# Performance work log

Hardware: AMD Instinct MI355X
Metric: run time of the kernel (lower is better)

Reference implementation:

```python
import jax, jax.numpy as jnp
import numpy as np

N, C, V, T = 256, 256, 25, 20
K = 3            # kernel_size
PAD = 1          # padding
O = 256          # out_channels
C4 = C // 4
EPS = 1e-5


def _bn(x, p, axes_shape):
    # p: (4, dim) = gamma, beta, running_mean, running_var (eval-mode BN)
    g, b, m, v = (p[i].reshape(axes_shape) for i in range(4))
    return (x - m) * (g / jnp.sqrt(v + EPS)) + b


def setup_inputs() -> dict:
    key = jax.random.key(0)
    ks = jax.random.split(key, 12)
    rn = lambda k, s, sc=0.05: jax.random.normal(k, s, jnp.float32) * sc
    bn = lambda k, d: jnp.stack([
        1.0 + 0.1 * jax.random.normal(jax.random.fold_in(k, 0), (d,), jnp.float32),  # gamma
        0.1 * jax.random.normal(jax.random.fold_in(k, 1), (d,), jnp.float32),        # beta
        0.1 * jax.random.normal(jax.random.fold_in(k, 2), (d,), jnp.float32),        # mean
        0.5 + jax.random.uniform(jax.random.fold_in(k, 3), (d,), jnp.float32),       # var
    ])
    return {
        "x": jax.random.normal(ks[0], (N, C, V, T), jnp.float32),
        "Wg1": rn(ks[1], (2 * T, T), 0.2),      # Linear T -> 2T (no bias)
        "Wg2": rn(ks[2], (K, 2 * T), 0.2),      # Linear 2T -> K (no bias)
        "Wl1": rn(ks[3], (C4, C, K)),           # Conv1d C -> C/4, kernel K
        "Wl2": rn(ks[4], (C, C4)),              # Conv1d C/4 -> C, kernel 1
        "Wc2": rn(ks[5], (O, C)),               # 1x1 Conv2d C -> O (no bias)
        "bng": bn(ks[6], 2 * T),
        "bnl": bn(ks[7], C4),
        "bn1p": bn(ks[8], C),
        "bn2p": bn(ks[9], O),
    }


def reference(x, Wg1, Wg2, Wl1, Wl2, Wc2, bng, bnl, bn1p, bn2p):
    n, c, v, t = x.shape
    new_x = jnp.transpose(x, (0, 1, 3, 2))            # (N, C, T, V)
    pooled = new_x.mean(axis=-1)                       # (N, C, T)  adaptive_avg_pool over V

    # --- G branch: per-(n,c) dynamic temporal kernel ---
    h = pooled.reshape(n * c, t) @ Wg1.T               # (NC, 2T)
    h = jax.nn.relu(_bn(h, bng, (1, 2 * t)))
    kern = jax.nn.softmax(h @ Wg2.T, axis=-1)          # (NC, K)
    kern = kern.reshape(n, c, K)

    # --- L branch: local temporal excitation ---
    l = jax.lax.conv_general_dilated(
        pooled, Wl1, window_strides=(1,), padding=[(K // 2, K // 2)],
        dimension_numbers=("NCH", "OIH", "NCH"))      # (N, C4, T)
    l = jax.nn.relu(_bn(l, bnl, (1, C4, 1)))
    l = jax.nn.sigmoid(jnp.einsum("oc,nct->not", Wl2, l))  # (N, C, T)
    new_x = new_x + l[..., None]                       # (N, C, T, V)

    # --- dynamic depthwise temporal conv (groups = N*C) ---
    padded = jnp.pad(new_x, ((0, 0), (0, 0), (PAD, PAD), (0, 0)))
    out = sum(kern[:, :, k, None, None] * padded[:, :, k:k + t, :] for k in range(K))

    out = jnp.transpose(out, (0, 1, 3, 2))             # (N, C, V, T)
    out = jax.nn.relu(_bn(out, bn1p, (1, c, 1, 1)))    # bn1 + relu; dropout in eval = identity
    out = jnp.einsum("oc,ncvt->novt", Wc2, out)        # 1x1 conv
    out = jax.nn.relu(_bn(out, bn2p, (1, O, 1, 1)))    # bn2 + relu
    return out
```

## Files before the change

### kernel.cpp

```cpp
#include <hip/hip_runtime.h>
#include <hip/hip_bf16.h>
#include <math.h>

#define N_ 256
#define C_ 256
#define V_ 25
#define T_ 20
#define C4_ 64
#define O_ 256
#define VT_ 500
#define EPS_ 1e-5f

typedef unsigned short ushort_t;
typedef short short8 __attribute__((ext_vector_type(8)));
typedef float f32x4 __attribute__((ext_vector_type(4)));

__device__ __forceinline__ ushort_t f2bf(float f) {
    unsigned int u = __builtin_bit_cast(unsigned int, f);
    unsigned int r = u + 0x7fffu + ((u >> 16) & 1u);
    return (ushort_t)(r >> 16);
}

__global__ __launch_bounds__(256) void k_pool(const float* __restrict__ x,
                                              float* __restrict__ pooled) {
    int idx = blockIdx.x * 256 + threadIdx.x;
    int t = idx % T_;
    int nc = idx / T_;
    const float* p = x + nc * (V_ * T_) + t;
    float s = 0.f;
#pragma unroll
    for (int v = 0; v < V_; ++v) s += p[v * T_];
    pooled[idx] = s * (1.0f / V_);
}

__global__ __launch_bounds__(256) void k_prep(const float* __restrict__ Wc2,
                                              ushort_t* __restrict__ wbf) {
    int i = blockIdx.x * 256 + threadIdx.x;
    wbf[i] = f2bf(Wc2[i]);
}

__global__ __launch_bounds__(256) void k_g(const float* __restrict__ Wg1,
                                           const float* __restrict__ Wg2,
                                           const float* __restrict__ bng,
                                           const float* __restrict__ pooled,
                                           float* __restrict__ kern) {
    __shared__ float wg1[800];
    __shared__ float wg2[120];
    __shared__ float sg[40], bg[40];
    int tid = threadIdx.x;
    for (int i = tid; i < 800; i += 256) wg1[i] = Wg1[i];
    if (tid < 120) wg2[tid] = Wg2[tid];
    if (tid < 40) {
        float g = bng[tid], b = bng[40 + tid];
        float m = bng[80 + tid], v = bng[120 + tid];
        float s = g * rsqrtf(v + EPS_);
        sg[tid] = s; bg[tid] = b - m * s;
    }
    __syncthreads();

    int nc = blockIdx.x * 256 + tid;
    const f32x4* pr = (const f32x4*)(pooled + nc * T_);
    float p[20];
#pragma unroll
    for (int q = 0; q < 5; ++q) {
        f32x4 v = pr[q];
        p[q*4+0] = v.x; p[q*4+1] = v.y; p[q*4+2] = v.z; p[q*4+3] = v.w;
    }
    float l0 = 0.f, l1 = 0.f, l2 = 0.f;
#pragma unroll 4
    for (int j = 0; j < 40; ++j) {
        float h = 0.f;
#pragma unroll
        for (int t = 0; t < 20; ++t) h = fmaf(wg1[j * 20 + t], p[t], h);
        h = fmaxf(fmaf(h, sg[j], bg[j]), 0.f);
        l0 = fmaf(wg2[j], h, l0);
        l1 = fmaf(wg2[40 + j], h, l1);
        l2 = fmaf(wg2[80 + j], h, l2);
    }
    float mx = fmaxf(l0, fmaxf(l1, l2));
    float e0 = __expf(l0 - mx), e1 = __expf(l1 - mx), e2 = __expf(l2 - mx);
    float inv = 1.f / (e0 + e1 + e2);
    float* kp = kern + nc * 3;
    kp[0] = e0 * inv; kp[1] = e1 * inv; kp[2] = e2 * inv;
}

__global__ __launch_bounds__(256) void k_l(const float* __restrict__ Wl1,
                                           const float* __restrict__ Wl2,
                                           const float* __restrict__ bnl,
                                           const float* __restrict__ pooled,
                                           float* __restrict__ l2out) {
    __shared__ float pp[C_][22];
    __shared__ float ls[C4_][20];
    __shared__ float sl[C4_], bl[C4_];
    int tid = threadIdx.x;
    int n = blockIdx.x;
    const float* pn = pooled + n * (C_ * T_);
    for (int i = tid; i < C_ * T_; i += 256) {
        int c = i / T_, t = i % T_;
        pp[c][t + 1] = pn[i];
    }
    pp[tid][0] = 0.f; pp[tid][21] = 0.f;
    if (tid < C4_) {
        float g = bnl[tid], b = bnl[64 + tid];
        float m = bnl[128 + tid], v = bnl[192 + tid];
        float s = g * rsqrtf(v + EPS_);
        sl[tid] = s; bl[tid] = b - m * s;
    }
    __syncthreads();
    {
        int c4 = tid >> 2;
        int t0 = (tid & 3) * 5;
        float acc0 = 0.f, acc1 = 0.f, acc2 = 0.f, acc3 = 0.f, acc4 = 0.f;
        const float* w = Wl1 + c4 * (C_ * 3);
        for (int c = 0; c < C_; ++c) {
            float w0 = w[c * 3 + 0];
            float w1 = w[c * 3 + 1];
            float w2 = w[c * 3 + 2];
            float a0 = pp[c][t0 + 0], a1 = pp[c][t0 + 1], a2 = pp[c][t0 + 2];
            float a3 = pp[c][t0 + 3], a4 = pp[c][t0 + 4], a5 = pp[c][t0 + 5];
            float a6 = pp[c][t0 + 6];
            acc0 = fmaf(w0, a0, fmaf(w1, a1, fmaf(w2, a2, acc0)));
            acc1 = fmaf(w0, a1, fmaf(w1, a2, fmaf(w2, a3, acc1)));
            acc2 = fmaf(w0, a2, fmaf(w1, a3, fmaf(w2, a4, acc2)));
            acc3 = fmaf(w0, a3, fmaf(w1, a4, fmaf(w2, a5, acc3)));
            acc4 = fmaf(w0, a4, fmaf(w1, a5, fmaf(w2, a6, acc4)));
        }
        float s = sl[c4], b = bl[c4];
        ls[c4][t0 + 0] = fmaxf(fmaf(acc0, s, b), 0.f);
        ls[c4][t0 + 1] = fmaxf(fmaf(acc1, s, b), 0.f);
        ls[c4][t0 + 2] = fmaxf(fmaf(acc2, s, b), 0.f);
        ls[c4][t0 + 3] = fmaxf(fmaf(acc3, s, b), 0.f);
        ls[c4][t0 + 4] = fmaxf(fmaf(acc4, s, b), 0.f);
    }
    __syncthreads();
    {
        int c = tid;
        float acc[20];
#pragma unroll
        for (int t = 0; t < 20; ++t) acc[t] = 0.f;
        const float* w = Wl2 + c * C4_;
        for (int c4 = 0; c4 < C4_; ++c4) {
            float wv = w[c4];
#pragma unroll
            for (int t = 0; t < 20; ++t) acc[t] = fmaf(wv, ls[c4][t], acc[t]);
        }
        float* o = l2out + n * (C_ * T_) + c * T_;
#pragma unroll
        for (int t = 0; t < 20; ++t) o[t] = 1.f / (1.f + __expf(-acc[t]));
    }
}

#define YSTRIDE 264

__global__ __launch_bounds__(256, 2) void k_main(const float* __restrict__ x,
                                                 const ushort_t* __restrict__ wbf,
                                                 const float* __restrict__ bn1p,
                                                 const float* __restrict__ bn2p,
                                                 const float* __restrict__ kern,
                                                 const float* __restrict__ l2ws,
                                                 float* __restrict__ out) {
    __shared__ __align__(16) ushort_t yT[112 * YSTRIDE];
    __shared__ float s2t[O_], b2t[O_];
    int tid = threadIdx.x;
    int n = blockIdx.y;
    int vblk = blockIdx.x;

    {
        int c = tid;
        float g1 = bn1p[c], be1 = bn1p[256 + c];
        float m1 = bn1p[512 + c], v1 = bn1p[768 + c];
        float s1 = g1 * rsqrtf(v1 + EPS_);
        float b1 = be1 - m1 * s1;
        float g2 = bn2p[c], be2 = bn2p[256 + c];
        float m2 = bn2p[512 + c], v2 = bn2p[768 + c];
        float s2 = g2 * rsqrtf(v2 + EPS_);
        s2t[c] = s2; b2t[c] = be2 - m2 * s2;

        const float* kp = kern + (n * C_ + c) * 3;
        float k0 = kp[0], k1 = kp[1], k2 = kp[2];
        float l2r[20];
        const f32x4* lp = (const f32x4*)(l2ws + (n * C_ + c) * T_);
#pragma unroll
        for (int q = 0; q < 5; ++q) {
            f32x4 v = lp[q];
            l2r[q*4+0] = v.x; l2r[q*4+1] = v.y; l2r[q*4+2] = v.z; l2r[q*4+3] = v.w;
        }
        const float* xp = x + ((n * C_ + c) * V_ + vblk * 5) * T_;
#pragma unroll
        for (int vl = 0; vl < 5; ++vl) {
            float a[22];
            a[0] = 0.f; a[21] = 0.f;
            const f32x4* xv = (const f32x4*)(xp + vl * T_);
#pragma unroll
            for (int q = 0; q < 5; ++q) {
                f32x4 u = xv[q];
                a[q*4 + 1] = u.x + l2r[q*4 + 0];
                a[q*4 + 2] = u.y + l2r[q*4 + 1];
                a[q*4 + 3] = u.z + l2r[q*4 + 2];
                a[q*4 + 4] = u.w + l2r[q*4 + 3];
            }
            ushort_t* yrow = yT + (vl * 20) * YSTRIDE + c;
#pragma unroll
            for (int t = 0; t < 20; ++t) {
                float z = fmaf(k0, a[t], fmaf(k1, a[t + 1], k2 * a[t + 2]));
                float y = fmaxf(fmaf(z, s1, b1), 0.f);
                yrow[t * YSTRIDE] = f2bf(y);
            }
        }
    }
    for (int i = tid; i < 12 * YSTRIDE; i += 256) yT[100 * YSTRIDE + i] = 0;
    __syncthreads();

    int lane = tid & 63;
    int wave = tid >> 6;
    int mrow = lane & 15;
    int kof = (lane >> 4) * 8;
    int obase = wave * 64;

    f32x4 acc[4][7];
#pragma unroll
    for (int mt = 0; mt < 4; ++mt)
#pragma unroll
        for (int ct = 0; ct < 7; ++ct) acc[mt][ct] = (f32x4){0.f, 0.f, 0.f, 0.f};

#pragma unroll 2
    for (int kk = 0; kk < C_; kk += 32) {
        short8 af[4];
        short8 bfr[7];
#pragma unroll
        for (int mt = 0; mt < 4; ++mt)
            af[mt] = *(const short8*)(wbf + (obase + mt * 16 + mrow) * C_ + kk + kof);
#pragma unroll
        for (int ct = 0; ct < 7; ++ct)
            bfr[ct] = *(const short8*)(yT + (ct * 16 + mrow) * YSTRIDE + kk + kof);
#pragma unroll
        for (int mt = 0; mt < 4; ++mt)
#pragma unroll
            for (int ct = 0; ct < 7; ++ct)
                acc[mt][ct] = __builtin_amdgcn_mfma_f32_16x16x32_bf16(af[mt], bfr[ct], acc[mt][ct], 0, 0, 0);
    }

    int prow = (lane >> 4) * 4;
    float* outn = out + n * (O_ * VT_);
#pragma unroll
    for (int ct = 0; ct < 7; ++ct) {
        int pl = ct * 16 + (lane & 15);
        if (pl < 100) {
            int p = vblk * 100 + pl;
#pragma unroll
            for (int mt = 0; mt < 4; ++mt) {
#pragma unroll
                for (int r = 0; r < 4; ++r) {
                    int o = obase + mt * 16 + prow + r;
                    float val = fmaxf(fmaf(acc[mt][ct][r], s2t[o], b2t[o]), 0.f);
                    outn[o * VT_ + p] = val;
                }
            }
        }
    }
}

extern "C" void kernel_launch(void* const* d_in, const int* in_sizes, int n_in,
                              void* d_out, int out_size, void* d_ws, size_t ws_size,
                              hipStream_t stream) {
    const float* x   = (const float*)d_in[0];
    const float* Wg1 = (const float*)d_in[1];
    const float* Wg2 = (const float*)d_in[2];
    const float* Wl1 = (const float*)d_in[3];
    const float* Wl2 = (const float*)d_in[4];
    const float* Wc2 = (const float*)d_in[5];
    const float* bng = (const float*)d_in[6];
    const float* bnl = (const float*)d_in[7];
    const float* bn1p = (const float*)d_in[8];
    const float* bn2p = (const float*)d_in[9];
    float* out = (float*)d_out;

    float* ws = (float*)d_ws;
    float* pooled = ws;
    float* kern   = ws + 1310720;
    float* l2ws   = ws + 1310720 + 196608;
    ushort_t* wbf = (ushort_t*)(ws + 1310720 + 196608 + 1310720);

    k_pool<<<dim3((N_ * C_ * T_) / 256), dim3(256), 0, stream>>>(x, pooled);
    k_prep<<<dim3((O_ * C_) / 256), dim3(256), 0, stream>>>(Wc2, wbf);
    k_g<<<dim3(N_ * C_ / 256), dim3(256), 0, stream>>>(Wg1, Wg2, bng, pooled, kern);
    k_l<<<dim3(N_), dim3(256), 0, stream>>>(Wl1, Wl2, bnl, pooled, l2ws);
    k_main<<<dim3(5, N_), dim3(256), 0, stream>>>(x, wbf, bn1p, bn2p, kern, l2ws, out);
}
```

Before: 371.8 us.

## Fuse pooling, G and L branches into one front kernel emitting bf16 x

Merges the pooling, weight prep, G-branch and L-branch kernels into a single per-batch front kernel that pools x directly into shared memory, which removes the pooled workspace round trip and three launches. The front kernel also writes a bf16 copy of x, which k_main reads instead of the fp32 input, halving its input traffic. In exchange x is read twice in fp32 by the front kernel and the bf16 copy is written once. The front stage now runs only 257 blocks, which may underfill the GPU. Rounding x to bf16 before the l add and the temporal conv also adds precision loss.

Result: slower. 385.4 us (+3.7%).

```diff
diff --git a/kernel.cpp b/kernel.cpp
--- a/kernel.cpp
+++ b/kernel.cpp
@@ -12,42 +12,54 @@
 #define EPS_ 1e-5f
 
 typedef unsigned short ushort_t;
+typedef unsigned short us4 __attribute__((ext_vector_type(4)));
 typedef short short8 __attribute__((ext_vector_type(8)));
 typedef float f32x4 __attribute__((ext_vector_type(4)));
 
+__device__ __forceinline__ float bf2f(ushort_t u) {
+    unsigned int v = ((unsigned int)u) << 16;
+    return __builtin_bit_cast(float, v);
+}
 __device__ __forceinline__ ushort_t f2bf(float f) {
     unsigned int u = __builtin_bit_cast(unsigned int, f);
     unsigned int r = u + 0x7fffu + ((u >> 16) & 1u);
     return (ushort_t)(r >> 16);
 }
 
-__global__ __launch_bounds__(256) void k_pool(const float* __restrict__ x,
-                                              float* __restrict__ pooled) {
-    int idx = blockIdx.x * 256 + threadIdx.x;
-    int t = idx % T_;
-    int nc = idx / T_;
-    const float* p = x + nc * (V_ * T_) + t;
-    float s = 0.f;
-#pragma unroll
-    for (int v = 0; v < V_; ++v) s += p[v * T_];
-    pooled[idx] = s * (1.0f / V_);
-}
-
-__global__ __launch_bounds__(256) void k_prep(const float* __restrict__ Wc2,
-                                              ushort_t* __restrict__ wbf) {
-    int i = blockIdx.x * 256 + threadIdx.x;
-    wbf[i] = f2bf(Wc2[i]);
-}
-
-__global__ __launch_bounds__(256) void k_g(const float* __restrict__ Wg1,
-                                           const float* __restrict__ Wg2,
-                                           const float* __restrict__ bng,
-                                           const float* __restrict__ pooled,
-                                           float* __restrict__ kern) {
+__global__ __launch_bounds__(256) void k_front(const float* __restrict__ x,
+                                               const float* __restrict__ Wg1,
+                                               const float* __restrict__ Wg2,
+                                               const float* __restrict__ Wl1,
+                                               const float* __restrict__ Wl2,
+                                               const float* __restrict__ Wc2,
+                                               const float* __restrict__ bng,
+                                               const float* __restrict__ bnl,
+                                               float* __restrict__ kern,
+                                               float* __restrict__ l2out,
+                                               ushort_t* __restrict__ xbf,
+                                               ushort_t* __restrict__ wbf) {
+    int tid = threadIdx.x;
+    if (blockIdx.x == 256) {
+        const f32x4* src = (const f32x4*)Wc2;
+        us4* dst = (us4*)wbf;
+        for (int i = tid; i < 16384; i += 256) {
+            f32x4 v = src[i];
+            us4 o; o.x = f2bf(v.x); o.y = f2bf(v.y); o.z = f2bf(v.z); o.w = f2bf(v.w);
+            dst[i] = o;
+        }
+        return;
+    }
+
+    __shared__ float pp[C_][22];
     __shared__ float wg1[800];
     __shared__ float wg2[120];
     __shared__ float sg[40], bg[40];
-    int tid = threadIdx.x;
+    __shared__ float ls[C4_][20];
+    __shared__ float sl[C4_], bl[C4_];
+
+    int n = blockIdx.x;
+    const float* xn = x + n * (C_ * V_ * T_);
+
     for (int i = tid; i < 800; i += 256) wg1[i] = Wg1[i];
     if (tid < 120) wg2[tid] = Wg2[tid];
     if (tid < 40) {
@@ -56,57 +68,46 @@
         float s = g * rsqrtf(v + EPS_);
         sg[tid] = s; bg[tid] = b - m * s;
     }
-    __syncthreads();
-
-    int nc = blockIdx.x * 256 + tid;
-    const f32x4* pr = (const f32x4*)(pooled + nc * T_);
-    float p[20];
-#pragma unroll
-    for (int q = 0; q < 5; ++q) {
-        f32x4 v = pr[q];
-        p[q*4+0] = v.x; p[q*4+1] = v.y; p[q*4+2] = v.z; p[q*4+3] = v.w;
-    }
-    float l0 = 0.f, l1 = 0.f, l2 = 0.f;
-#pragma unroll 4
-    for (int j = 0; j < 40; ++j) {
-        float h = 0.f;
-#pragma unroll
-        for (int t = 0; t < 20; ++t) h = fmaf(wg1[j * 20 + t], p[t], h);
-        h = fmaxf(fmaf(h, sg[j], bg[j]), 0.f);
-        l0 = fmaf(wg2[j], h, l0);
-        l1 = fmaf(wg2[40 + j], h, l1);
-        l2 = fmaf(wg2[80 + j], h, l2);
-    }
-    float mx = fmaxf(l0, fmaxf(l1, l2));
-    float e0 = __expf(l0 - mx), e1 = __expf(l1 - mx), e2 = __expf(l2 - mx);
-    float inv = 1.f / (e0 + e1 + e2);
-    float* kp = kern + nc * 3;
-    kp[0] = e0 * inv; kp[1] = e1 * inv; kp[2] = e2 * inv;
-}
-
-__global__ __launch_bounds__(256) void k_l(const float* __restrict__ Wl1,
-                                           const float* __restrict__ Wl2,
-                                           const float* __restrict__ bnl,
-                                           const float* __restrict__ pooled,
-                                           float* __restrict__ l2out) {
-    __shared__ float pp[C_][22];
-    __shared__ float ls[C4_][20];
-    __shared__ float sl[C4_], bl[C4_];
-    int tid = threadIdx.x;
-    int n = blockIdx.x;
-    const float* pn = pooled + n * (C_ * T_);
-    for (int i = tid; i < C_ * T_; i += 256) {
-        int c = i / T_, t = i % T_;
-        pp[c][t + 1] = pn[i];
-    }
-    pp[tid][0] = 0.f; pp[tid][21] = 0.f;
     if (tid < C4_) {
         float g = bnl[tid], b = bnl[64 + tid];
         float m = bnl[128 + tid], v = bnl[192 + tid];
         float s = g * rsqrtf(v + EPS_);
         sl[tid] = s; bl[tid] = b - m * s;
     }
+    for (int i = tid; i < C_ * T_; i += 256) {
+        int c = i / T_, t = i % T_;
+        const float* p = xn + c * (V_ * T_) + t;
+        float s = 0.f;
+#pragma unroll
+        for (int v = 0; v < V_; ++v) s += p[v * T_];
+        pp[c][t + 1] = s * (1.0f / V_);
+    }
+    pp[tid][0] = 0.f; pp[tid][21] = 0.f;
     __syncthreads();
+
+    {
+        int c = tid;
+        float p[20];
+#pragma unroll
+        for (int t = 0; t < 20; ++t) p[t] = pp[c][t + 1];
+        float l0 = 0.f, l1 = 0.f, l2 = 0.f;
+#pragma unroll 4
+        for (int j = 0; j < 40; ++j) {
+            float h = 0.f;
+#pragma unroll
+            for (int t = 0; t < 20; ++t) h = fmaf(wg1[j * 20 + t], p[t], h);
+            h = fmaxf(fmaf(h, sg[j], bg[j]), 0.f);
+            l0 = fmaf(wg2[j], h, l0);
+            l1 = fmaf(wg2[40 + j], h, l1);
+            l2 = fmaf(wg2[80 + j], h, l2);
+        }
+        float mx = fmaxf(l0, fmaxf(l1, l2));
+        float e0 = __expf(l0 - mx), e1 = __expf(l1 - mx), e2 = __expf(l2 - mx);
+        float inv = 1.f / (e0 + e1 + e2);
+        float* kp = kern + (n * C_ + c) * 3;
+        kp[0] = e0 * inv; kp[1] = e1 * inv; kp[2] = e2 * inv;
+    }
+
     {
         int c4 = tid >> 2;
         int t0 = (tid & 3) * 5;
@@ -133,6 +134,7 @@
         ls[c4][t0 + 4] = fmaxf(fmaf(acc4, s, b), 0.f);
     }
     __syncthreads();
+
     {
         int c = tid;
         float acc[20];
@@ -148,11 +150,21 @@
 #pragma unroll
         for (int t = 0; t < 20; ++t) o[t] = 1.f / (1.f + __expf(-acc[t]));
     }
+
+    {
+        const f32x4* src = (const f32x4*)xn;
+        us4* dst = (us4*)(xbf + n * (C_ * V_ * T_));
+        for (int i = tid; i < (C_ * V_ * T_) / 4; i += 256) {
+            f32x4 v = src[i];
+            us4 o; o.x = f2bf(v.x); o.y = f2bf(v.y); o.z = f2bf(v.z); o.w = f2bf(v.w);
+            dst[i] = o;
+        }
+    }
 }
 
 #define YSTRIDE 264
 
-__global__ __launch_bounds__(256, 2) void k_main(const float* __restrict__ x,
+__global__ __launch_bounds__(256, 2) void k_main(const ushort_t* __restrict__ xbf,
                                                  const ushort_t* __restrict__ wbf,
                                                  const float* __restrict__ bn1p,
                                                  const float* __restrict__ bn2p,
@@ -185,19 +197,19 @@
             f32x4 v = lp[q];
             l2r[q*4+0] = v.x; l2r[q*4+1] = v.y; l2r[q*4+2] = v.z; l2r[q*4+3] = v.w;
         }
-        const float* xp = x + ((n * C_ + c) * V_ + vblk * 5) * T_;
+        const ushort_t* xp = xbf + ((n * C_ + c) * V_ + vblk * 5) * T_;
 #pragma unroll
         for (int vl = 0; vl < 5; ++vl) {
             float a[22];
             a[0] = 0.f; a[21] = 0.f;
-            const f32x4* xv = (const f32x4*)(xp + vl * T_);
+            const us4* xv = (const us4*)(xp + vl * T_);
 #pragma unroll
             for (int q = 0; q < 5; ++q) {
-                f32x4 u = xv[q];
-                a[q*4 + 1] = u.x + l2r[q*4 + 0];
-                a[q*4 + 2] = u.y + l2r[q*4 + 1];
-                a[q*4 + 3] = u.z + l2r[q*4 + 2];
-                a[q*4 + 4] = u.w + l2r[q*4 + 3];
+                us4 u = xv[q];
+                a[q*4 + 1] = bf2f(u.x) + l2r[q*4 + 0];
+                a[q*4 + 2] = bf2f(u.y) + l2r[q*4 + 1];
+                a[q*4 + 3] = bf2f(u.z) + l2r[q*4 + 2];
+                a[q*4 + 4] = bf2f(u.w) + l2r[q*4 + 3];
             }
             ushort_t* yrow = yT + (vl * 20) * YSTRIDE + c;
 #pragma unroll
@@ -276,14 +288,12 @@
     float* out = (float*)d_out;
 
     float* ws = (float*)d_ws;
-    float* pooled = ws;
-    float* kern   = ws + 1310720;
-    float* l2ws   = ws + 1310720 + 196608;
-    ushort_t* wbf = (ushort_t*)(ws + 1310720 + 196608 + 1310720);
-
-    k_pool<<<dim3((N_ * C_ * T_) / 256), dim3(256), 0, stream>>>(x, pooled);
-    k_prep<<<dim3((O_ * C_) / 256), dim3(256), 0, stream>>>(Wc2, wbf);
-    k_g<<<dim3(N_ * C_ / 256), dim3(256), 0, stream>>>(Wg1, Wg2, bng, pooled, kern);
-    k_l<<<dim3(N_), dim3(256), 0, stream>>>(Wl1, Wl2, bnl, pooled, l2ws);
-    k_main<<<dim3(5, N_), dim3(256), 0, stream>>>(x, wbf, bn1p, bn2p, kern, l2ws, out);
-}
+    float* kern  = ws;
+    float* l2ws  = ws + 196608;
+    ushort_t* wbf = (ushort_t*)(ws + 196608 + 1310720);
+    ushort_t* xbf = wbf + 65536;
+
+    k_front<<<dim3(257), dim3(256), 0, stream>>>(x, Wg1, Wg2, Wl1, Wl2, Wc2, bng, bnl,
+                                                 kern, l2ws, xbf, wbf);
+    k_main<<<dim3(5, N_), dim3(256), 0, stream>>>(xbf, wbf, bn1p, bn2p, kern, l2ws, out);
+}
```

## Fuse pooling, G/L branches and main GEMM into one per-sample mega kernel

Applied to the files above, without the earlier changes.

Merges the pool, G-branch, L-branch and main kernels into a single kernel with one block per sample. Pooled values, dynamic kernels and the sigmoid excitation stay in shared memory and registers instead of making workspace round trips. The block loops over the five V-blocks and stages the output through shared memory so it can be written as coalesced 16-byte vectors. The cost is a grid of only 256 blocks with launch bounds allowing one block per CU, so parallelism and latency hiding drop, and each block now runs the serial G/L prologue before its GEMM work.

Measured after the change: 374.2 us. About the same (+0.6%).

```diff
diff --git a/kernel.cpp b/kernel.cpp
--- a/kernel.cpp
+++ b/kernel.cpp
@@ -12,6 +12,7 @@
 #define EPS_ 1e-5f
 
 typedef unsigned short ushort_t;
+typedef unsigned short us4 __attribute__((ext_vector_type(4)));
 typedef short short8 __attribute__((ext_vector_type(8)));
 typedef float f32x4 __attribute__((ext_vector_type(4)));
 
@@ -21,33 +22,45 @@
     return (ushort_t)(r >> 16);
 }
 
-__global__ __launch_bounds__(256) void k_pool(const float* __restrict__ x,
-                                              float* __restrict__ pooled) {
-    int idx = blockIdx.x * 256 + threadIdx.x;
-    int t = idx % T_;
-    int nc = idx / T_;
-    const float* p = x + nc * (V_ * T_) + t;
-    float s = 0.f;
-#pragma unroll
-    for (int v = 0; v < V_; ++v) s += p[v * T_];
-    pooled[idx] = s * (1.0f / V_);
-}
-
 __global__ __launch_bounds__(256) void k_prep(const float* __restrict__ Wc2,
                                               ushort_t* __restrict__ wbf) {
     int i = blockIdx.x * 256 + threadIdx.x;
-    wbf[i] = f2bf(Wc2[i]);
-}
-
-__global__ __launch_bounds__(256) void k_g(const float* __restrict__ Wg1,
-                                           const float* __restrict__ Wg2,
-                                           const float* __restrict__ bng,
-                                           const float* __restrict__ pooled,
-                                           float* __restrict__ kern) {
-    __shared__ float wg1[800];
-    __shared__ float wg2[120];
-    __shared__ float sg[40], bg[40];
+    f32x4 v = ((const f32x4*)Wc2)[i];
+    us4 o; o.x = f2bf(v.x); o.y = f2bf(v.y); o.z = f2bf(v.z); o.w = f2bf(v.w);
+    ((us4*)wbf)[i] = o;
+}
+
+#define YSTRIDE 264
+
+__global__ __launch_bounds__(256, 1) void k_mega(const float* __restrict__ x,
+                                                 const ushort_t* __restrict__ wbf,
+                                                 const float* __restrict__ Wg1,
+                                                 const float* __restrict__ Wg2,
+                                                 const float* __restrict__ Wl1,
+                                                 const float* __restrict__ Wl2,
+                                                 const float* __restrict__ bng,
+                                                 const float* __restrict__ bnl,
+                                                 const float* __restrict__ bn1p,
+                                                 const float* __restrict__ bn2p,
+                                                 float* __restrict__ out) {
+    __shared__ __align__(16) char smem[61184];
+    float (*pp)[22] = (float(*)[22])(smem);
+    float* wg1 = (float*)(smem + 22528);
+    float* wg2 = (float*)(smem + 25728);
+    float* sg  = (float*)(smem + 26208);
+    float* bg  = (float*)(smem + 26368);
+    float (*ls)[20] = (float(*)[20])(smem + 26528);
+    float* sl  = (float*)(smem + 31648);
+    float* bl  = (float*)(smem + 31904);
+    ushort_t* yT = (ushort_t*)(smem);
+    float* outs  = (float*)(smem);
+    float* s2t = (float*)(smem + 59136);
+    float* b2t = (float*)(smem + 60160);
+
     int tid = threadIdx.x;
+    int n = blockIdx.x;
+    const float* xn = x + n * (C_ * V_ * T_);
+
     for (int i = tid; i < 800; i += 256) wg1[i] = Wg1[i];
     if (tid < 120) wg2[tid] = Wg2[tid];
     if (tid < 40) {
@@ -56,62 +69,80 @@
         float s = g * rsqrtf(v + EPS_);
         sg[tid] = s; bg[tid] = b - m * s;
     }
-    __syncthreads();
-
-    int nc = blockIdx.x * 256 + tid;
-    const f32x4* pr = (const f32x4*)(pooled + nc * T_);
-    float p[20];
-#pragma unroll
-    for (int q = 0; q < 5; ++q) {
-        f32x4 v = pr[q];
-        p[q*4+0] = v.x; p[q*4+1] = v.y; p[q*4+2] = v.z; p[q*4+3] = v.w;
-    }
-    float l0 = 0.f, l1 = 0.f, l2 = 0.f;
-#pragma unroll 4
-    for (int j = 0; j < 40; ++j) {
-        float h = 0.f;
-#pragma unroll
-        for (int t = 0; t < 20; ++t) h = fmaf(wg1[j * 20 + t], p[t], h);
-        h = fmaxf(fmaf(h, sg[j], bg[j]), 0.f);
-        l0 = fmaf(wg2[j], h, l0);
-        l1 = fmaf(wg2[40 + j], h, l1);
-        l2 = fmaf(wg2[80 + j], h, l2);
-    }
-    float mx = fmaxf(l0, fmaxf(l1, l2));
-    float e0 = __expf(l0 - mx), e1 = __expf(l1 - mx), e2 = __expf(l2 - mx);
-    float inv = 1.f / (e0 + e1 + e2);
-    float* kp = kern + nc * 3;
-    kp[0] = e0 * inv; kp[1] = e1 * inv; kp[2] = e2 * inv;
-}
-
-__global__ __launch_bounds__(256) void k_l(const float* __restrict__ Wl1,
-                                           const float* __restrict__ Wl2,
-                                           const float* __restrict__ bnl,
-                                           const float* __restrict__ pooled,
-                                           float* __restrict__ l2out) {
-    __shared__ float pp[C_][22];
-    __shared__ float ls[C4_][20];
-    __shared__ float sl[C4_], bl[C4_];
-    int tid = threadIdx.x;
-    int n = blockIdx.x;
-    const float* pn = pooled + n * (C_ * T_);
-    for (int i = tid; i < C_ * T_; i += 256) {
-        int c = i / T_, t = i % T_;
-        pp[c][t + 1] = pn[i];
-    }
-    pp[tid][0] = 0.f; pp[tid][21] = 0.f;
     if (tid < C4_) {
         float g = bnl[tid], b = bnl[64 + tid];
         float m = bnl[128 + tid], v = bnl[192 + tid];
         float s = g * rsqrtf(v + EPS_);
         sl[tid] = s; bl[tid] = b - m * s;
     }
+
+    {
+        f32x4 pacc[5];
+        const float* pbase[5];
+        int pc[5], ptq[5];
+#pragma unroll
+        for (int k = 0; k < 5; ++k) {
+            int s = tid + 256 * k;
+            pc[k] = s / 5; ptq[k] = s % 5;
+            pbase[k] = xn + pc[k] * (V_ * T_) + ptq[k] * 4;
+            pacc[k] = (f32x4){0.f, 0.f, 0.f, 0.f};
+        }
+#pragma unroll 5
+        for (int v = 0; v < V_; ++v) {
+#pragma unroll
+            for (int k = 0; k < 5; ++k)
+                pacc[k] += *(const f32x4*)(pbase[k] + v * T_);
+        }
+#pragma unroll
+        for (int k = 0; k < 5; ++k) {
+            int c = pc[k], t1 = ptq[k] * 4 + 1;
+            pp[c][t1 + 0] = pacc[k].x * 0.04f;
+            pp[c][t1 + 1] = pacc[k].y * 0.04f;
+            pp[c][t1 + 2] = pacc[k].z * 0.04f;
+            pp[c][t1 + 3] = pacc[k].w * 0.04f;
+        }
+        pp[tid][0] = 0.f; pp[tid][21] = 0.f;
+    }
     __syncthreads();
+
+    float k0, k1, k2, s1, b1;
+    {
+        int c = tid;
+        float p[20];
+#pragma unroll
+        for (int t = 0; t < 20; ++t) p[t] = pp[c][t + 1];
+        float l0 = 0.f, l1 = 0.f, l2 = 0.f;
+#pragma unroll 4
+        for (int j = 0; j < 40; ++j) {
+            float h = 0.f;
+#pragma unroll
+            for (int t = 0; t < 20; ++t) h = fmaf(wg1[j * 20 + t], p[t], h);
+            h = fmaxf(fmaf(h, sg[j], bg[j]), 0.f);
+            l0 = fmaf(wg2[j], h, l0);
+            l1 = fmaf(wg2[40 + j], h, l1);
+            l2 = fmaf(wg2[80 + j], h, l2);
+        }
+        float mx = fmaxf(l0, fmaxf(l1, l2));
+        float e0 = __expf(l0 - mx), e1 = __expf(l1 - mx), e2 = __expf(l2 - mx);
+        float inv = 1.f / (e0 + e1 + e2);
+        k0 = e0 * inv; k1 = e1 * inv; k2 = e2 * inv;
+
+        float g1 = bn1p[c], be1 = bn1p[256 + c];
+        float m1 = bn1p[512 + c], v1 = bn1p[768 + c];
+        s1 = g1 * rsqrtf(v1 + EPS_);
+        b1 = be1 - m1 * s1;
+        float g2 = bn2p[c], be2 = bn2p[256 + c];
+        float m2 = bn2p[512 + c], v2 = bn2p[768 + c];
+        float s2 = g2 * rsqrtf(v2 + EPS_);
+        s2t[c] = s2; b2t[c] = be2 - m2 * s2;
+    }
+
     {
         int c4 = tid >> 2;
         int t0 = (tid & 3) * 5;
         float acc0 = 0.f, acc1 = 0.f, acc2 = 0.f, acc3 = 0.f, acc4 = 0.f;
         const float* w = Wl1 + c4 * (C_ * 3);
+#pragma unroll 8
         for (int c = 0; c < C_; ++c) {
             float w0 = w[c * 3 + 0];
             float w1 = w[c * 3 + 1];
@@ -133,129 +164,111 @@
         ls[c4][t0 + 4] = fmaxf(fmaf(acc4, s, b), 0.f);
     }
     __syncthreads();
+
+    float l2r[20];
     {
         int c = tid;
-        float acc[20];
-#pragma unroll
-        for (int t = 0; t < 20; ++t) acc[t] = 0.f;
+#pragma unroll
+        for (int t = 0; t < 20; ++t) l2r[t] = 0.f;
         const float* w = Wl2 + c * C4_;
+#pragma unroll 4
         for (int c4 = 0; c4 < C4_; ++c4) {
             float wv = w[c4];
 #pragma unroll
-            for (int t = 0; t < 20; ++t) acc[t] = fmaf(wv, ls[c4][t], acc[t]);
-        }
-        float* o = l2out + n * (C_ * T_) + c * T_;
-#pragma unroll
-        for (int t = 0; t < 20; ++t) o[t] = 1.f / (1.f + __expf(-acc[t]));
-    }
-}
-
-#define YSTRIDE 264
-
-__global__ __launch_bounds__(256, 2) void k_main(const float* __restrict__ x,
-                                                 const ushort_t* __restrict__ wbf,
-                                                 const float* __restrict__ bn1p,
-                                                 const float* __restrict__ bn2p,
-                                                 const float* __restrict__ kern,
-                                                 const float* __restrict__ l2ws,
-                                                 float* __restrict__ out) {
-    __shared__ __align__(16) ushort_t yT[112 * YSTRIDE];
-    __shared__ float s2t[O_], b2t[O_];
-    int tid = threadIdx.x;
-    int n = blockIdx.y;
-    int vblk = blockIdx.x;
-
-    {
-        int c = tid;
-        float g1 = bn1p[c], be1 = bn1p[256 + c];
-        float m1 = bn1p[512 + c], v1 = bn1p[768 + c];
-        float s1 = g1 * rsqrtf(v1 + EPS_);
-        float b1 = be1 - m1 * s1;
-        float g2 = bn2p[c], be2 = bn2p[256 + c];
-        float m2 = bn2p[512 + c], v2 = bn2p[768 + c];
-        float s2 = g2 * rsqrtf(v2 + EPS_);
-        s2t[c] = s2; b2t[c] = be2 - m2 * s2;
-
-        const float* kp = kern + (n * C_ + c) * 3;
-        float k0 = kp[0], k1 = kp[1], k2 = kp[2];
-        float l2r[20];
-        const f32x4* lp = (const f32x4*)(l2ws + (n * C_ + c) * T_);
-#pragma unroll
-        for (int q = 0; q < 5; ++q) {
-            f32x4 v = lp[q];
-            l2r[q*4+0] = v.x; l2r[q*4+1] = v.y; l2r[q*4+2] = v.z; l2r[q*4+3] = v.w;
-        }
-        const float* xp = x + ((n * C_ + c) * V_ + vblk * 5) * T_;
-#pragma unroll
-        for (int vl = 0; vl < 5; ++vl) {
-            float a[22];
-            a[0] = 0.f; a[21] = 0.f;
-            const f32x4* xv = (const f32x4*)(xp + vl * T_);
-#pragma unroll
-            for (int q = 0; q < 5; ++q) {
-                f32x4 u = xv[q];
-                a[q*4 + 1] = u.x + l2r[q*4 + 0];
-                a[q*4 + 2] = u.y + l2r[q*4 + 1];
-                a[q*4 + 3] = u.z + l2r[q*4 + 2];
-                a[q*4 + 4] = u.w + l2r[q*4 + 3];
-            }
-            ushort_t* yrow = yT + (vl * 20) * YSTRIDE + c;
-#pragma unroll
-            for (int t = 0; t < 20; ++t) {
-                float z = fmaf(k0, a[t], fmaf(k1, a[t + 1], k2 * a[t + 2]));
-                float y = fmaxf(fmaf(z, s1, b1), 0.f);
-                yrow[t * YSTRIDE] = f2bf(y);
-            }
-        }
-    }
-    for (int i = tid; i < 12 * YSTRIDE; i += 256) yT[100 * YSTRIDE + i] = 0;
+            for (int t = 0; t < 20; ++t) l2r[t] = fmaf(wv, ls[c4][t], l2r[t]);
+        }
+#pragma unroll
+        for (int t = 0; t < 20; ++t) l2r[t] = 1.f / (1.f + __expf(-l2r[t]));
+    }
     __syncthreads();
 
     int lane = tid & 63;
     int wave = tid >> 6;
     int mrow = lane & 15;
     int kof = (lane >> 4) * 8;
+    int prow = (lane >> 4) * 4;
     int obase = wave * 64;
-
-    f32x4 acc[4][7];
-#pragma unroll
-    for (int mt = 0; mt < 4; ++mt)
-#pragma unroll
-        for (int ct = 0; ct < 7; ++ct) acc[mt][ct] = (f32x4){0.f, 0.f, 0.f, 0.f};
-
-#pragma unroll 2
-    for (int kk = 0; kk < C_; kk += 32) {
-        short8 af[4];
-        short8 bfr[7];
-#pragma unroll
-        for (int mt = 0; mt < 4; ++mt)
-            af[mt] = *(const short8*)(wbf + (obase + mt * 16 + mrow) * C_ + kk + kof);
-#pragma unroll
-        for (int ct = 0; ct < 7; ++ct)
-            bfr[ct] = *(const short8*)(yT + (ct * 16 + mrow) * YSTRIDE + kk + kof);
-#pragma unroll
-        for (int mt = 0; mt < 4; ++mt)
-#pragma unroll
-            for (int ct = 0; ct < 7; ++ct)
-                acc[mt][ct] = __builtin_amdgcn_mfma_f32_16x16x32_bf16(af[mt], bfr[ct], acc[mt][ct], 0, 0, 0);
-    }
-
-    int prow = (lane >> 4) * 4;
     float* outn = out + n * (O_ * VT_);
-#pragma unroll
-    for (int ct = 0; ct < 7; ++ct) {
-        int pl = ct * 16 + (lane & 15);
-        if (pl < 100) {
-            int p = vblk * 100 + pl;
-#pragma unroll
-            for (int mt = 0; mt < 4; ++mt) {
-#pragma unroll
-                for (int r = 0; r < 4; ++r) {
-                    int o = obase + mt * 16 + prow + r;
-                    float val = fmaxf(fmaf(acc[mt][ct][r], s2t[o], b2t[o]), 0.f);
-                    outn[o * VT_ + p] = val;
+
+    for (int vblk = 0; vblk < 5; ++vblk) {
+        {
+            int c = tid;
+            const float* xp = xn + (c * V_ + vblk * 5) * T_;
+#pragma unroll
+            for (int vl = 0; vl < 5; ++vl) {
+                float a[22];
+                a[0] = 0.f; a[21] = 0.f;
+                const f32x4* xv = (const f32x4*)(xp + vl * T_);
+#pragma unroll
+                for (int q = 0; q < 5; ++q) {
+                    f32x4 u = xv[q];
+                    a[q*4 + 1] = u.x + l2r[q*4 + 0];
+                    a[q*4 + 2] = u.y + l2r[q*4 + 1];
+                    a[q*4 + 3] = u.z + l2r[q*4 + 2];
+                    a[q*4 + 4] = u.w + l2r[q*4 + 3];
+                }
+                ushort_t* yrow = yT + (vl * 20) * YSTRIDE + c;
+#pragma unroll
+                for (int t = 0; t < 20; ++t) {
+                    float z = fmaf(k0, a[t], fmaf(k1, a[t + 1], k2 * a[t + 2]));
+                    float y = fmaxf(fmaf(z, s1, b1), 0.f);
+                    yrow[t * YSTRIDE] = f2bf(y);
                 }
             }
+        }
+        for (int i = tid; i < 12 * YSTRIDE; i += 256) yT[100 * YSTRIDE + i] = 0;
+        __syncthreads();
+
+        f32x4 acc[4][7];
+#pragma unroll
+        for (int mt = 0; mt < 4; ++mt)
+#pragma unroll
+            for (int ct = 0; ct < 7; ++ct) acc[mt][ct] = (f32x4){0.f, 0.f, 0.f, 0.f};
+
+#pragma unroll 2
+        for (int kk = 0; kk < C_; kk += 32) {
+            short8 af[4];
+            short8 bfr[7];
+#pragma unroll
+            for (int mt = 0; mt < 4; ++mt)
+                af[mt] = *(const short8*)(wbf + (obase + mt * 16 + mrow) * C_ + kk + kof);
+#pragma unroll
+            for (int ct = 0; ct < 7; ++ct)
+                bfr[ct] = *(const short8*)(yT + (ct * 16 + mrow) * YSTRIDE + kk + kof);
+#pragma unroll
+            for (int mt = 0; mt < 4; ++mt)
+#pragma unroll
+                for (int ct = 0; ct < 7; ++ct)
+                    acc[mt][ct] = __builtin_amdgcn_mfma_f32_16x16x32_bf16(af[mt], bfr[ct], acc[mt][ct], 0, 0, 0);
+        }
+        __syncthreads();
+
+#pragma unroll
+        for (int P = 0; P < 2; ++P) {
+#pragma unroll
+            for (int mtl = 0; mtl < 2; ++mtl) {
+                int mt = 2 * P + mtl;
+#pragma unroll
+                for (int ct = 0; ct < 7; ++ct) {
+                    int pl = ct * 16 + mrow;
+                    if (pl < 100) {
+#pragma unroll
+                        for (int r = 0; r < 4; ++r) {
+                            int og = obase + mt * 16 + prow + r;
+                            int oo = wave * 32 + mtl * 16 + prow + r;
+                            outs[oo * 100 + pl] =
+                                fmaxf(fmaf(acc[mt][ct][r], s2t[og], b2t[og]), 0.f);
+                        }
+                    }
+                }
+            }
+            __syncthreads();
+            for (int i = tid; i < 3200; i += 256) {
+                int oo = i / 25, col = i % 25;
+                int og = (oo >> 5) * 64 + P * 32 + (oo & 31);
+                *(f32x4*)(outn + og * VT_ + vblk * 100 + col * 4) = ((const f32x4*)outs)[i];
+            }
+            __syncthreads();
         }
     }
 }
@@ -275,15 +288,9 @@
     const float* bn2p = (const float*)d_in[9];
     float* out = (float*)d_out;
 
-    float* ws = (float*)d_ws;
-    float* pooled = ws;
-    float* kern   = ws + 1310720;
-    float* l2ws   = ws + 1310720 + 196608;
-    ushort_t* wbf = (ushort_t*)(ws + 1310720 + 196608 + 1310720);
-
-    k_pool<<<dim3((N_ * C_ * T_) / 256), dim3(256), 0, stream>>>(x, pooled);
-    k_prep<<<dim3((O_ * C_) / 256), dim3(256), 0, stream>>>(Wc2, wbf);
-    k_g<<<dim3(N_ * C_ / 256), dim3(256), 0, stream>>>(Wg1, Wg2, bng, pooled, kern);
-    k_l<<<dim3(N_), dim3(256), 0, stream>>>(Wl1, Wl2, bnl, pooled, l2ws);
-    k_main<<<dim3(5, N_), dim3(256), 0, stream>>>(x, wbf, bn1p, bn2p, kern, l2ws, out);
-}
+    ushort_t* wbf = (ushort_t*)d_ws;
+
+    k_prep<<<dim3(64), dim3(256), 0, stream>>>(Wc2, wbf);
+    k_mega<<<dim3(N_), dim3(256), 0, stream>>>(x, wbf, Wg1, Wg2, Wl1, Wl2,
+                                               bng, bnl, bn1p, bn2p, out);
+}
```
